# Kernel optimization log

Hardware: AMD Instinct MI355X
Metric: run time of the kernel (lower is better)

The kernel has to match this reference:

```python
import jax, jax.numpy as jnp
import numpy as np

N, E, D, L, R = 100000, 500000, 128, 2, 10
EPS = 1e-5  # BatchNorm1d default eps


def setup_inputs() -> dict:
    key = jax.random.key(0)
    ks = jax.random.split(key, 10)
    return {
        "in_node_emb": jax.random.normal(ks[0], (N, D), jnp.float32),
        "in_rel_emb": jax.random.normal(ks[1], (R, D), jnp.float32),
        "w_in": jax.random.normal(ks[2], (L, D, D), jnp.float32) * 0.05,
        "w_out": jax.random.normal(ks[3], (L, D, D), jnp.float32) * 0.05,
        "w_loop": jax.random.normal(ks[4], (L, D, D), jnp.float32) * 0.05,
        "w_rel": jax.random.normal(ks[5], (L, D, D), jnp.float32) * 0.05,
        "loop_rel": jax.random.normal(ks[6], (L, 1, D), jnp.float32) * 0.05,
        "bias": jnp.zeros((L, D), jnp.float32),
        "edge_src": jax.random.randint(ks[7], (E,), 0, N),
        "edge_dst": jax.random.randint(ks[8], (E,), 0, N),
        "edge_type": jax.random.randint(ks[9], (E,), 0, R),
    }


def _gcn_forward(in_node_emb, in_rel_emb, w_in, w_out, w_loop, w_rel, loop_rel,
                 bias, edge_src, edge_dst, edge_type):
    x, r = in_node_emb, in_rel_emb
    ones_e = jnp.ones((E,), in_node_emb.dtype)
    for l in range(L):
        rel = jnp.concatenate([r, loop_rel[l]], axis=0)  # [R+1, D]; last row = self-loop relation
        rel_e = rel[edge_type]                            # [E, D] per-edge relation embedding

        def directed_msg(row, col, w):
            # gather -> compose ('mult') -> linear -> degree norm -> scatter-add at row
            comp = x[col] * rel_e                         # [E, D]
            m = comp @ w                                  # [E, D]
            deg = jnp.zeros((N,), x.dtype).at[row].add(ones_e)
            dinv = jnp.where(deg > 0, jax.lax.rsqrt(deg), 0.0)
            m = m * (dinv[row] * dinv[col])[:, None]
            return jnp.zeros((N, D), x.dtype).at[row].add(m)

        in_res = directed_msg(edge_src, edge_dst, w_in[l])   # original direction (src<-dst msgs)
        out_res = directed_msg(edge_dst, edge_src, w_out[l]) # mirrored direction
        loop_res = (x * loop_rel[l]) @ w_loop[l]             # self-loop (no norm)
        out = (in_res + out_res + loop_res) * (1.0 / 3.0) + bias[l]
        # BatchNorm1d over nodes, batch statistics, gamma=1 beta=0
        mean = out.mean(axis=0)
        var = out.var(axis=0)
        out = (out - mean) * jax.lax.rsqrt(var + EPS)
        x = jnp.tanh(out)
        r = (rel @ w_rel[l])[:-1]                            # transform rels, drop loop row
    return x, r


def reference(in_node_emb, in_rel_emb, w_in, w_out, w_loop, w_rel, loop_rel,
              bias, edge_src, edge_dst, edge_type):
    return _gcn_forward(in_node_emb, in_rel_emb, w_in, w_out, w_loop, w_rel,
                        loop_rel, bias, edge_src, edge_dst, edge_type)
```

## Files before the change

### kernel.cpp

```cpp
#include <hip/hip_runtime.h>
#include <math.h>

#define Nn 100000
#define Ee 500000
#define Dd 128
#define Rr 10
#define ND (Nn * Dd)
#define SCAN_CHUNK 1024
#define NBLK ((Nn + SCAN_CHUNK - 1) / SCAN_CHUNK)
#define LDK 136
#define EPSF 1e-5f
#define XBLK (ND / 8 / 256)

typedef _Float16 half_t;
typedef __attribute__((ext_vector_type(8))) _Float16 half8;
typedef __attribute__((ext_vector_type(4))) float f32x4;
typedef unsigned short ushort;
typedef unsigned int uint;
typedef unsigned long long u64;

union H4 { u64 u; _Float16 h[4]; };
union H8 { uint4 q; _Float16 h[8]; };

__device__ __forceinline__ void atomAddF(float* p, float v) {
    unsafeAtomicAdd(p, v);
}

__global__ void kzeroi(int* p, int n) {
    int i = blockIdx.x * blockDim.x + threadIdx.x;
    int stride = gridDim.x * blockDim.x;
    for (; i < n; i += stride) p[i] = 0;
}

__global__ void khist(const int* __restrict__ src, const int* __restrict__ dst,
                      int* cnt_s, int* cnt_d, int ne) {
    int e = blockIdx.x * blockDim.x + threadIdx.x;
    if (e < ne) {
        atomicAdd(&cnt_s[src[e]], 1);
        atomicAdd(&cnt_d[dst[e]], 1);
    }
}

__global__ __launch_bounds__(256) void kscan1(
    const int* __restrict__ cnt_s, const int* __restrict__ cnt_d,
    int* off_s, int* off_d, int* bsum_s, int* bsum_d,
    float* dinv_s, float* dinv_d) {
    int dir = blockIdx.x >= NBLK;
    int lb = blockIdx.x - dir * NBLK;
    const int* cnt = dir ? cnt_d : cnt_s;
    int* off = dir ? off_d : off_s;
    int* bsum = dir ? bsum_d : bsum_s;
    float* dinv = dir ? dinv_d : dinv_s;
    __shared__ int s[256];
    int tid = threadIdx.x;
    int base = lb * SCAN_CHUNK + tid * 4;
    int v[4], sum = 0;
#pragma unroll
    for (int q = 0; q < 4; q++) {
        int c = (base + q < Nn) ? cnt[base + q] : 0;
        v[q] = c;
        sum += c;
        if (base + q < Nn) dinv[base + q] = (c > 0) ? rsqrtf((float)c) : 0.f;
    }
    s[tid] = sum;
    __syncthreads();
#pragma unroll
    for (int ofs = 1; ofs < 256; ofs <<= 1) {
        int t = (tid >= ofs) ? s[tid - ofs] : 0;
        __syncthreads();
        s[tid] += t;
        __syncthreads();
    }
    if (tid == 255) bsum[lb] = s[255];
    int run = s[tid] - sum;
#pragma unroll
    for (int q = 0; q < 4; q++) {
        if (base + q < Nn) off[base + q] = run;
        run += v[q];
    }
}

__global__ __launch_bounds__(128) void kscan2(int* bsum_s, int* bsum_d,
                                              int* off_s, int* off_d) {
    int dir = blockIdx.x;
    int* bsum = dir ? bsum_d : bsum_s;
    int* off = dir ? off_d : off_s;
    __shared__ int s[128];
    int tid = threadIdx.x;
    int v = (tid < NBLK) ? bsum[tid] : 0;
    s[tid] = v;
    __syncthreads();
#pragma unroll
    for (int ofs = 1; ofs < 128; ofs <<= 1) {
        int t = (tid >= ofs) ? s[tid - ofs] : 0;
        __syncthreads();
        s[tid] += t;
        __syncthreads();
    }
    if (tid < NBLK) bsum[tid] = s[tid] - v;
    if (tid == 127) off[Nn] = s[127];
}

__global__ void kscan3(int* off_s, int* off_d, const int* __restrict__ bsum_s,
                       const int* __restrict__ bsum_d, int* cur_s, int* cur_d) {
    int idx = blockIdx.x * blockDim.x + threadIdx.x;
    if (idx >= 2 * Nn) return;
    int dir = idx >= Nn;
    int i = idx - dir * Nn;
    int* off = dir ? off_d : off_s;
    const int* bsum = dir ? bsum_d : bsum_s;
    int* cur = dir ? cur_d : cur_s;
    int o = off[i] + bsum[i >> 10];
    off[i] = o;
    cur[i] = o;
}

__global__ void kscatter(const int* __restrict__ src, const int* __restrict__ dst,
                         const int* __restrict__ typ,
                         const float* __restrict__ dinv_s, const float* __restrict__ dinv_d,
                         int* cur_s, int* cur_d,
                         u64* rec_s, u64* rec_d, int ne) {
    int e = blockIdx.x * blockDim.x + threadIdx.x;
    if (e >= ne) return;
    int s = src[e], d = dst[e], t = typ[e];
    int ps = atomicAdd(&cur_s[s], 1);
    rec_s[ps] = (u64)(uint)((d << 4) | t) |
                ((u64)__float_as_uint(dinv_s[s] * dinv_s[d]) << 32);
    int pd = atomicAdd(&cur_d[d], 1);
    rec_d[pd] = (u64)(uint)((s << 4) | t) |
                ((u64)__float_as_uint(dinv_d[d] * dinv_d[s]) << 32);
}

__global__ __launch_bounds__(256) void kprep(
    const float* __restrict__ x, const float* __restrict__ lr0,
    const float* __restrict__ w_in, const float* __restrict__ w_out,
    const float* __restrict__ w_loop, const float* __restrict__ w_rel,
    const float* __restrict__ r0,
    half_t* __restrict__ xb, half_t* __restrict__ xlb,
    half_t* __restrict__ Wt, float* __restrict__ rel0p, float* __restrict__ rel1p,
    float* __restrict__ r2out) {
    int blk = blockIdx.x;
    int tid = threadIdx.x;
    if (blk < XBLK) {
        int idx = blk * 256 + tid;
        int base = idx * 8;
        int k = base & 127;
        float4 v0 = *(const float4*)(x + base);
        float4 v1 = *(const float4*)(x + base + 4);
        float4 l0 = *(const float4*)(lr0 + k);
        float4 l1 = *(const float4*)(lr0 + k + 4);
        H8 xo, xl;
        xo.h[0] = (half_t)v0.x; xo.h[1] = (half_t)v0.y; xo.h[2] = (half_t)v0.z; xo.h[3] = (half_t)v0.w;
        xo.h[4] = (half_t)v1.x; xo.h[5] = (half_t)v1.y; xo.h[6] = (half_t)v1.z; xo.h[7] = (half_t)v1.w;
        xl.h[0] = (half_t)(v0.x * l0.x); xl.h[1] = (half_t)(v0.y * l0.y);
        xl.h[2] = (half_t)(v0.z * l0.z); xl.h[3] = (half_t)(v0.w * l0.w);
        xl.h[4] = (half_t)(v1.x * l1.x); xl.h[5] = (half_t)(v1.y * l1.y);
        xl.h[6] = (half_t)(v1.z * l1.z); xl.h[7] = (half_t)(v1.w * l1.w);
        *(uint4*)(xb + base) = xo.q;
        *(uint4*)(xlb + base) = xl.q;
    } else if (blk < XBLK + 384) {
        int idx = (blk - XBLK) * 256 + tid;
        int l = idx >= 49152;
        int rem = idx - l * 49152;
        int p = rem >> 14, ri = rem & 16383;
        int n = ri >> 7, k = ri & 127;
        const float* W = (p == 0) ? (w_in + l * 16384)
                       : ((p == 1) ? (w_out + l * 16384) : (w_loop + l * 16384));
        Wt[idx] = (half_t)W[k * 128 + n];
    } else if (blk == XBLK + 384) {
        __shared__ float sr[Rr * Dd];
        for (int i = tid; i < Rr * Dd; i += 256) sr[i] = r0[i];
        __syncthreads();
        for (int ph = 0; ph < 2; ph++) {
            const float* w = w_rel + ph * 16384;
            float o[5];
#pragma unroll
            for (int q = 0; q < 5; q++) {
                int oi = tid + q * 256;
                int row = oi >> 7, j = oi & 127;
                float acc = 0.f;
                for (int k = 0; k < 128; k++) acc += sr[row * 128 + k] * w[k * 128 + j];
                o[q] = acc;
            }
            __syncthreads();
            float* dst = ph ? r2out : rel1p;
#pragma unroll
            for (int q = 0; q < 5; q++) {
                int oi = tid + q * 256;
                sr[oi] = o[q];
                dst[oi] = o[q];
            }
            __syncthreads();
        }
        for (int i = Rr * Dd + tid; i < 16 * Dd; i += 256) rel1p[i] = 0.f;
    } else {
        for (int i = tid; i < 16 * Dd; i += 256) rel0p[i] = (i < Rr * Dd) ? r0[i] : 0.f;
    }
}

__global__ __launch_bounds__(256) void kgather(
    const int* __restrict__ off_s, const u64* __restrict__ rec_s,
    const int* __restrict__ off_d, const u64* __restrict__ rec_d,
    const half_t* __restrict__ xb, const float* __restrict__ relp,
    half_t* __restrict__ aggin, half_t* __restrict__ aggout, int gb) {
    int blk = blockIdx.x;
    const int* off; const u64* rec; half_t* agg;
    if (blk < gb) { off = off_s; rec = rec_s; agg = aggin; }
    else { blk -= gb; off = off_d; rec = rec_d; agg = aggout; }
    int wv = threadIdx.x >> 6;
    int lane = threadIdx.x & 63;
    int hf = lane >> 5;
    int hl = lane & 31;
    int node = blk * 8 + wv * 2 + hf;
    bool valid = node < Nn;
    int nodec = valid ? node : (Nn - 1);
    int b = off[nodec];
    int e = off[nodec + 1];
    int n_it = valid ? (e - b) : 0;
    int other = __shfl(n_it, lane ^ 32, 64);
    int mx = n_it > other ? n_it : other;

    const u64* x4 = (const u64*)xb;
    const float4* r4 = (const float4*)relp;
    float a0 = 0.f, a1 = 0.f, a2 = 0.f, a3 = 0.f;

    for (int it0 = 0; it0 < mx; it0 += 8) {
        u64 rr[8];
#pragma unroll
        for (int q = 0; q < 8; q++) rr[q] = rec[b + it0 + q];
        H4 xv[8]; float4 rl[8]; float wq[8];
#pragma unroll
        for (int q = 0; q < 8; q++) {
            uint p = (uint)rr[q];
            uint nmb = (uint)(rr[q] >> 32);
            bool c = (it0 + q) < n_it;
            wq[q] = c ? __uint_as_float(nmb) : 0.f;
            int xi = c ? (int)(p >> 4) : 0;
            xv[q].u = x4[(size_t)xi * 32 + hl];
            rl[q] = r4[(p & 15u) * 32 + hl];
        }
#pragma unroll
        for (int q = 0; q < 8; q++) {
            a0 += (float)xv[q].h[0] * rl[q].x * wq[q];
            a1 += (float)xv[q].h[1] * rl[q].y * wq[q];
            a2 += (float)xv[q].h[2] * rl[q].z * wq[q];
            a3 += (float)xv[q].h[3] * rl[q].w * wq[q];
        }
    }
    if (valid) {
        H4 o;
        o.h[0] = (half_t)a0; o.h[1] = (half_t)a1;
        o.h[2] = (half_t)a2; o.h[3] = (half_t)a3;
        ((u64*)agg)[(size_t)node * 32 + hl] = o.u;
    }
}

__global__ __launch_bounds__(256) void kmm(
    const half_t* __restrict__ aggin, const half_t* __restrict__ aggout,
    const half_t* __restrict__ xlb, const half_t* __restrict__ Wt,
    const float* __restrict__ bias, half_t* __restrict__ out,
    float* colsum, float* colsumsq) {
    __shared__ half_t sW[128 * LDK];
    const int tid = threadIdx.x;
    const int wv = tid >> 6;
    const int lane = tid & 63;
    const int col = lane & 15;
    const int quad = lane >> 4;
    const int m0 = blockIdx.x * 128;
    const int rowbase = m0 + wv * 32;

    f32x4 acc[2][8];
#pragma unroll
    for (int m = 0; m < 2; m++)
#pragma unroll
        for (int j = 0; j < 8; j++) acc[m][j] = (f32x4){0.f, 0.f, 0.f, 0.f};

    const half_t* Ap[3] = {aggin, aggout, xlb};
    int r0 = rowbase + col;
    int r1 = r0 + 16;
    int r0c = (r0 < Nn) ? r0 : (Nn - 1);
    int r1c = (r1 < Nn) ? r1 : (Nn - 1);

    for (int p = 0; p < 3; p++) {
        __syncthreads();
        {
            const half8* Wg = (const half8*)(Wt + p * 16384);
#pragma unroll
            for (int i = 0; i < 8; i++) {
                int c = tid + i * 256;
                int n = c >> 4, ko = (c & 15) * 8;
                *(half8*)(sW + n * LDK + ko) = Wg[c];
            }
        }
        __syncthreads();
        const half_t* A = Ap[p];
#pragma unroll
        for (int s = 0; s < 4; s++) {
            int ko = s * 32 + quad * 8;
            half8 va0 = *(const half8*)(A + r0c * Dd + ko);
            half8 va1 = *(const half8*)(A + r1c * Dd + ko);
#pragma unroll
            for (int j = 0; j < 8; j++) {
                half8 vb = *(const half8*)(sW + (j * 16 + col) * LDK + ko);
                acc[0][j] = __builtin_amdgcn_mfma_f32_16x16x32_f16(va0, vb, acc[0][j], 0, 0, 0);
                acc[1][j] = __builtin_amdgcn_mfma_f32_16x16x32_f16(va1, vb, acc[1][j], 0, 0, 0);
            }
        }
    }

    const float inv3 = 1.f / 3.f;
    float bcol[8], sum[8], ssq[8];
#pragma unroll
    for (int j = 0; j < 8; j++) {
        bcol[j] = bias[j * 16 + col];
        sum[j] = 0.f; ssq[j] = 0.f;
    }
#pragma unroll
    for (int m = 0; m < 2; m++) {
        int rb = rowbase + m * 16;
        if (rb < Nn) {
#pragma unroll
            for (int j = 0; j < 8; j++) {
#pragma unroll
                for (int r = 0; r < 4; r++) {
                    float v = acc[m][j][r] * inv3 + bcol[j];
                    out[(rb + quad * 4 + r) * Dd + j * 16 + col] = (half_t)v;
                    sum[j] += v;
                    ssq[j] += v * v;
                }
            }
        }
    }
#pragma unroll
    for (int j = 0; j < 8; j++) {
        sum[j] += __shfl_xor(sum[j], 16, 64);
        sum[j] += __shfl_xor(sum[j], 32, 64);
        ssq[j] += __shfl_xor(ssq[j], 16, 64);
        ssq[j] += __shfl_xor(ssq[j], 32, 64);
    }
    __syncthreads();
    float* sred = (float*)sW;
    if (quad == 0) {
#pragma unroll
        for (int j = 0; j < 8; j++) {
            sred[wv * 128 + j * 16 + col] = sum[j];
            sred[512 + wv * 128 + j * 16 + col] = ssq[j];
        }
    }
    __syncthreads();
    if (tid < 128) {
        float s = 0.f, s2 = 0.f;
#pragma unroll
        for (int w = 0; w < 4; w++) {
            s += sred[w * 128 + tid];
            s2 += sred[512 + w * 128 + tid];
        }
        atomAddF(&colsum[tid], s);
        atomAddF(&colsumsq[tid], s2);
    }
}

__global__ __launch_bounds__(256) void knorm0(const half_t* __restrict__ outh,
                                              const float* __restrict__ colsum,
                                              const float* __restrict__ colsumsq,
                                              const float* __restrict__ lr,
                                              half_t* __restrict__ xb,
                                              half_t* __restrict__ xlb) {
    __shared__ float sm[128], srs[128];
    int tid = threadIdx.x;
    if (tid < 128) {
        float m = colsum[tid] * (1.f / (float)Nn);
        float v = colsumsq[tid] * (1.f / (float)Nn) - m * m;
        sm[tid] = m;
        srs[tid] = rsqrtf(v + EPSF);
    }
    __syncthreads();
    int idx = blockIdx.x * 256 + tid;
    int base = idx * 8;
    int k = base & 127;
    H8 v; v.q = *(const uint4*)(outh + base);
    H8 xo, xl;
#pragma unroll
    for (int q = 0; q < 8; q++) {
        float t = tanhf(((float)v.h[q] - sm[k + q]) * srs[k + q]);
        xo.h[q] = (half_t)t;
        xl.h[q] = (half_t)(t * lr[k + q]);
    }
    *(uint4*)(xb + base) = xo.q;
    *(uint4*)(xlb + base) = xl.q;
}

__global__ __launch_bounds__(256) void knorm1(const half_t* __restrict__ outh,
                                              const float* __restrict__ colsum,
                                              const float* __restrict__ colsumsq,
                                              float* __restrict__ xn) {
    __shared__ float sm[128], srs[128];
    int tid = threadIdx.x;
    if (tid < 128) {
        float m = colsum[tid] * (1.f / (float)Nn);
        float v = colsumsq[tid] * (1.f / (float)Nn) - m * m;
        sm[tid] = m;
        srs[tid] = rsqrtf(v + EPSF);
    }
    __syncthreads();
    int idx = blockIdx.x * 256 + tid;
    int base = idx * 8;
    int k = base & 127;
    H8 v; v.q = *(const uint4*)(outh + base);
    float4 o0, o1;
    o0.x = tanhf(((float)v.h[0] - sm[k + 0]) * srs[k + 0]);
    o0.y = tanhf(((float)v.h[1] - sm[k + 1]) * srs[k + 1]);
    o0.z = tanhf(((float)v.h[2] - sm[k + 2]) * srs[k + 2]);
    o0.w = tanhf(((float)v.h[3] - sm[k + 3]) * srs[k + 3]);
    o1.x = tanhf(((float)v.h[4] - sm[k + 4]) * srs[k + 4]);
    o1.y = tanhf(((float)v.h[5] - sm[k + 5]) * srs[k + 5]);
    o1.z = tanhf(((float)v.h[6] - sm[k + 6]) * srs[k + 6]);
    o1.w = tanhf(((float)v.h[7] - sm[k + 7]) * srs[k + 7]);
    *(float4*)(xn + base) = o0;
    *(float4*)(xn + base + 4) = o1;
}

extern "C" void kernel_launch(void* const* d_in, const int* in_sizes, int n_in,
                              void* d_out, int out_size, void* d_ws, size_t ws_size,
                              hipStream_t stream) {
    const float* x0      = (const float*)d_in[0];
    const float* r0      = (const float*)d_in[1];
    const float* w_in    = (const float*)d_in[2];
    const float* w_out   = (const float*)d_in[3];
    const float* w_loop  = (const float*)d_in[4];
    const float* w_rel   = (const float*)d_in[5];
    const float* looprel = (const float*)d_in[6];
    const float* bias    = (const float*)d_in[7];
    const int* esrc = (const int*)d_in[8];
    const int* edst = (const int*)d_in[9];
    const int* etyp = (const int*)d_in[10];
    float* outp = (float*)d_out;

    half_t* us = (half_t*)d_ws;
    half_t* aggin_h  = us;
    half_t* aggout_h = us + (size_t)ND;
    half_t* xb       = us + 2 * (size_t)ND;
    half_t* xlb      = us + 3 * (size_t)ND;
    half_t* outh     = us + 4 * (size_t)ND;
    half_t* Wt       = us + 5 * (size_t)ND;
    u64* rec_s = (u64*)(us + 5 * (size_t)ND + 2 * 49152);
    u64* rec_d = rec_s + (Ee + 64);
    float* fp = (float*)(rec_d + (Ee + 64));
    float* dinv_s  = fp;   fp += Nn;
    float* dinv_d  = fp;   fp += Nn;
    float* rel0p   = fp;   fp += 16 * Dd;
    float* rel1p   = fp;   fp += 16 * Dd;
    int* ip = (int*)fp;
    int* cnt_s  = ip;  ip += Nn;
    int* cnt_d  = ip;  ip += Nn;
    float* colsumA = (float*)ip;  ip += 2 * Dd;
    float* colsumB = (float*)ip;  ip += 2 * Dd;
    int* off_s  = ip;  ip += Nn + 1;
    int* off_d  = ip;  ip += Nn + 1;
    int* cur_s  = ip;  ip += Nn;
    int* cur_d  = ip;  ip += Nn;
    int* bsum_s = ip;  ip += 128;
    int* bsum_d = ip;  ip += 128;

    kzeroi<<<256, 256, 0, stream>>>(cnt_s, 2 * Nn + 4 * Dd);
    khist<<<(Ee + 255) / 256, 256, 0, stream>>>(esrc, edst, cnt_s, cnt_d, Ee);
    kscan1<<<2 * NBLK, 256, 0, stream>>>(cnt_s, cnt_d, off_s, off_d, bsum_s, bsum_d,
                                         dinv_s, dinv_d);
    kscan2<<<2, 128, 0, stream>>>(bsum_s, bsum_d, off_s, off_d);
    kscan3<<<(2 * Nn + 255) / 256, 256, 0, stream>>>(off_s, off_d, bsum_s, bsum_d,
                                                     cur_s, cur_d);
    kscatter<<<(Ee + 255) / 256, 256, 0, stream>>>(esrc, edst, etyp, dinv_s, dinv_d,
                                                   cur_s, cur_d, rec_s, rec_d, Ee);
    kprep<<<XBLK + 384 + 2, 256, 0, stream>>>(
        x0, looprel, w_in, w_out, w_loop, w_rel, r0,
        xb, xlb, Wt, rel0p, rel1p, outp + (size_t)ND);

    const int gb = (Nn + 7) / 8;
    for (int l = 0; l < 2; l++) {
        const float* relp = l ? rel1p : rel0p;
        float* cs = l ? colsumB : colsumA;
        kgather<<<2 * gb, 256, 0, stream>>>(off_s, rec_s, off_d, rec_d,
                                            xb, relp, aggin_h, aggout_h, gb);
        kmm<<<(Nn + 127) / 128, 256, 0, stream>>>(aggin_h, aggout_h, xlb, Wt + l * 49152,
                                                  bias + l * Dd, outh, cs, cs + Dd);
        if (l == 0) {
            knorm0<<<ND / 8 / 256, 256, 0, stream>>>(outh, cs, cs + Dd, looprel + Dd, xb, xlb);
        } else {
            knorm1<<<ND / 8 / 256, 256, 0, stream>>>(outh, cs, cs + Dd, outp);
        }
    }
}
```

Baseline: 509.5 us.

## Use packed fp16 math and LDS relation table in edge gather kernel

The gather kernel now gives each node 16 lanes that load 16 bytes of fp16 features each, instead of 32 lanes loading 8 bytes. Relation embeddings are stored as fp16 and staged in shared memory. Products and accumulation are done with packed half2 arithmetic, and the edge loop is unrolled by two instead of batches of eight. This cuts gather instructions and relation-table global loads per edge. The cost is lower accuracy from fp16 accumulation of the weighted sums and less memory-level parallelism per lane.

```diff
diff --git a/kernel.cpp b/kernel.cpp
--- a/kernel.cpp
+++ b/kernel.cpp
@@ -13,14 +13,14 @@
 #define XBLK (ND / 8 / 256)
 
 typedef _Float16 half_t;
+typedef __attribute__((ext_vector_type(2))) _Float16 h2;
 typedef __attribute__((ext_vector_type(8))) _Float16 half8;
 typedef __attribute__((ext_vector_type(4))) float f32x4;
 typedef unsigned short ushort;
 typedef unsigned int uint;
 typedef unsigned long long u64;
 
-union H4 { u64 u; _Float16 h[4]; };
-union H8 { uint4 q; _Float16 h[8]; };
+union H8 { uint4 q; _Float16 h[8]; h2 p[4]; };
 
 __device__ __forceinline__ void atomAddF(float* p, float v) {
     unsafeAtomicAdd(p, v);
@@ -137,7 +137,7 @@
     const float* __restrict__ w_loop, const float* __restrict__ w_rel,
     const float* __restrict__ r0,
     half_t* __restrict__ xb, half_t* __restrict__ xlb,
-    half_t* __restrict__ Wt, float* __restrict__ rel0p, float* __restrict__ rel1p,
+    half_t* __restrict__ Wt, half_t* __restrict__ rel0p, half_t* __restrict__ rel1p,
     float* __restrict__ r2out) {
     int blk = blockIdx.x;
     int tid = threadIdx.x;
@@ -183,75 +183,87 @@
                 o[q] = acc;
             }
             __syncthreads();
-            float* dst = ph ? r2out : rel1p;
 #pragma unroll
             for (int q = 0; q < 5; q++) {
                 int oi = tid + q * 256;
                 sr[oi] = o[q];
-                dst[oi] = o[q];
+                if (ph == 0) rel1p[oi] = (half_t)o[q];
+                else r2out[oi] = o[q];
             }
             __syncthreads();
         }
-        for (int i = Rr * Dd + tid; i < 16 * Dd; i += 256) rel1p[i] = 0.f;
+        for (int i = Rr * Dd + tid; i < 16 * Dd; i += 256) rel1p[i] = (half_t)0.f;
     } else {
-        for (int i = tid; i < 16 * Dd; i += 256) rel0p[i] = (i < Rr * Dd) ? r0[i] : 0.f;
+        for (int i = tid; i < 16 * Dd; i += 256)
+            rel0p[i] = (i < Rr * Dd) ? (half_t)r0[i] : (half_t)0.f;
     }
 }
 
 __global__ __launch_bounds__(256) void kgather(
     const int* __restrict__ off_s, const u64* __restrict__ rec_s,
     const int* __restrict__ off_d, const u64* __restrict__ rec_d,
-    const half_t* __restrict__ xb, const float* __restrict__ relp,
+    const half_t* __restrict__ xb, const half_t* __restrict__ relp,
     half_t* __restrict__ aggin, half_t* __restrict__ aggout, int gb) {
+    __shared__ uint4 sRel[256];
+    sRel[threadIdx.x] = ((const uint4*)relp)[threadIdx.x];
+    __syncthreads();
+
     int blk = blockIdx.x;
     const int* off; const u64* rec; half_t* agg;
     if (blk < gb) { off = off_s; rec = rec_s; agg = aggin; }
     else { blk -= gb; off = off_d; rec = rec_d; agg = aggout; }
     int wv = threadIdx.x >> 6;
     int lane = threadIdx.x & 63;
-    int hf = lane >> 5;
-    int hl = lane & 31;
-    int node = blk * 8 + wv * 2 + hf;
+    int nq = lane >> 4;
+    int hl = lane & 15;
+    int node = blk * 16 + wv * 4 + nq;
     bool valid = node < Nn;
     int nodec = valid ? node : (Nn - 1);
     int b = off[nodec];
-    int e = off[nodec + 1];
-    int n_it = valid ? (e - b) : 0;
-    int other = __shfl(n_it, lane ^ 32, 64);
-    int mx = n_it > other ? n_it : other;
-
-    const u64* x4 = (const u64*)xb;
-    const float4* r4 = (const float4*)relp;
-    float a0 = 0.f, a1 = 0.f, a2 = 0.f, a3 = 0.f;
-
-    for (int it0 = 0; it0 < mx; it0 += 8) {
-        u64 rr[8];
-#pragma unroll
-        for (int q = 0; q < 8; q++) rr[q] = rec[b + it0 + q];
-        H4 xv[8]; float4 rl[8]; float wq[8];
-#pragma unroll
-        for (int q = 0; q < 8; q++) {
-            uint p = (uint)rr[q];
-            uint nmb = (uint)(rr[q] >> 32);
-            bool c = (it0 + q) < n_it;
-            wq[q] = c ? __uint_as_float(nmb) : 0.f;
-            int xi = c ? (int)(p >> 4) : 0;
-            xv[q].u = x4[(size_t)xi * 32 + hl];
-            rl[q] = r4[(p & 15u) * 32 + hl];
-        }
-#pragma unroll
-        for (int q = 0; q < 8; q++) {
-            a0 += (float)xv[q].h[0] * rl[q].x * wq[q];
-            a1 += (float)xv[q].h[1] * rl[q].y * wq[q];
-            a2 += (float)xv[q].h[2] * rl[q].z * wq[q];
-            a3 += (float)xv[q].h[3] * rl[q].w * wq[q];
-        }
+    int n_it = valid ? (off[nodec + 1] - b) : 0;
+
+    const uint4* x16 = (const uint4*)xb;
+    h2 acc0 = {(half_t)0.f, (half_t)0.f}, acc1 = acc0, acc2 = acc0, acc3 = acc0;
+
+    int it = 0;
+    for (; it + 1 < n_it; it += 2) {
+        u64 rr0 = rec[b + it];
+        u64 rr1 = rec[b + it + 1];
+        uint p0 = (uint)rr0, p1 = (uint)rr1;
+        H8 xv0, xv1, rv0, rv1;
+        xv0.q = x16[(size_t)(p0 >> 4) * 16 + hl];
+        xv1.q = x16[(size_t)(p1 >> 4) * 16 + hl];
+        rv0.q = sRel[(p0 & 15u) * 16 + hl];
+        rv1.q = sRel[(p1 & 15u) * 16 + hl];
+        half_t w0h = (half_t)__uint_as_float((uint)(rr0 >> 32));
+        half_t w1h = (half_t)__uint_as_float((uint)(rr1 >> 32));
+        h2 w0 = {w0h, w0h}, w1 = {w1h, w1h};
+        acc0 += (xv0.p[0] * rv0.p[0]) * w0;
+        acc1 += (xv0.p[1] * rv0.p[1]) * w0;
+        acc2 += (xv0.p[2] * rv0.p[2]) * w0;
+        acc3 += (xv0.p[3] * rv0.p[3]) * w0;
+        acc0 += (xv1.p[0] * rv1.p[0]) * w1;
+        acc1 += (xv1.p[1] * rv1.p[1]) * w1;
+        acc2 += (xv1.p[2] * rv1.p[2]) * w1;
+        acc3 += (xv1.p[3] * rv1.p[3]) * w1;
+    }
+    if (it < n_it) {
+        u64 rr0 = rec[b + it];
+        uint p0 = (uint)rr0;
+        H8 xv0, rv0;
+        xv0.q = x16[(size_t)(p0 >> 4) * 16 + hl];
+        rv0.q = sRel[(p0 & 15u) * 16 + hl];
+        half_t w0h = (half_t)__uint_as_float((uint)(rr0 >> 32));
+        h2 w0 = {w0h, w0h};
+        acc0 += (xv0.p[0] * rv0.p[0]) * w0;
+        acc1 += (xv0.p[1] * rv0.p[1]) * w0;
+        acc2 += (xv0.p[2] * rv0.p[2]) * w0;
+        acc3 += (xv0.p[3] * rv0.p[3]) * w0;
     }
     if (valid) {
-        H4 o;
-        o.h[0] = (half_t)a0; o.h[1] = (half_t)a1;
-        o.h[2] = (half_t)a2; o.h[3] = (half_t)a3;
-        ((u64*)agg)[(size_t)node * 32 + hl] = o.u;
+        H8 o;
+        o.p[0] = acc0; o.p[1] = acc1; o.p[2] = acc2; o.p[3] = acc3;
+        ((uint4*)agg)[(size_t)node * 16 + hl] = o.q;
     }
 }
 
@@ -443,13 +455,13 @@
     half_t* xlb      = us + 3 * (size_t)ND;
     half_t* outh     = us + 4 * (size_t)ND;
     half_t* Wt       = us + 5 * (size_t)ND;
-    u64* rec_s = (u64*)(us + 5 * (size_t)ND + 2 * 49152);
+    half_t* rel0p    = Wt + 2 * 49152;
+    half_t* rel1p    = rel0p + 16 * Dd;
+    u64* rec_s = (u64*)(rel1p + 16 * Dd);
     u64* rec_d = rec_s + (Ee + 64);
     float* fp = (float*)(rec_d + (Ee + 64));
     float* dinv_s  = fp;   fp += Nn;
     float* dinv_d  = fp;   fp += Nn;
-    float* rel0p   = fp;   fp += 16 * Dd;
-    float* rel1p   = fp;   fp += 16 * Dd;
     int* ip = (int*)fp;
     int* cnt_s  = ip;  ip += Nn;
     int* cnt_d  = ip;  ip += Nn;
@@ -475,9 +487,9 @@
         x0, looprel, w_in, w_out, w_loop, w_rel, r0,
         xb, xlb, Wt, rel0p, rel1p, outp + (size_t)ND);
 
-    const int gb = (Nn + 7) / 8;
+    const int gb = (Nn + 15) / 16;
     for (int l = 0; l < 2; l++) {
-        const float* relp = l ? rel1p : rel0p;
+        const half_t* relp = l ? rel1p : rel0p;
         float* cs = l ? colsumB : colsumA;
         kgather<<<2 * gb, 256, 0, stream>>>(off_s, rec_s, off_d, rec_d,
                                             xb, relp, aggin_h, aggout_h, gb);
```

After: 453.0 us. -11.1%, faster.
